# Performance work log

Measured on AMD Instinct MI355X. Metric: run time of the kernel, lower is better.

The kernel has to match this reference:

```python
import jax, jax.numpy as jnp
import numpy as np

B = 8192
W = 48            # target-net width
P = 4849          # flat param size of target MLP(1->48->48->48->1)
HW = 96           # hypernet width = 2*W
STEPS = 20
LR = 0.1
B1, B2, EPS = 0.9, 0.999, 1e-8


def setup_inputs() -> dict:
    key = jax.random.key(0)
    ks = jax.random.split(key, 6)
    x = jax.random.normal(ks[0], (B, 1), dtype=jnp.float32)
    c = jax.random.normal(ks[1], (B, 1), dtype=jnp.float32)
    # hypernet params (Linear(2,96) -> relu -> Linear(96,4849)), He-ish scaling
    hw1 = jax.random.normal(ks[2], (HW, 2), dtype=jnp.float32) / jnp.sqrt(2.0)
    hb1 = jax.random.normal(ks[3], (HW,), dtype=jnp.float32) * 0.1
    hw2 = jax.random.normal(ks[4], (P, HW), dtype=jnp.float32) / jnp.sqrt(float(HW))
    hb2 = jax.random.normal(ks[5], (P,), dtype=jnp.float32) * 0.1
    return {"x": x, "c": c, "hw1": hw1, "hb1": hb1, "hw2": hw2, "hb2": hb2}


def _target_apply(p, y):
    # unflatten per tree_flatten order: (w,b) per Linear layer of MLP(1,48,48,48,1)
    w0 = p[0:48].reshape(W, 1);      b0 = p[48:96]
    w1 = p[96:2400].reshape(W, W);   b1 = p[2400:2448]
    w2 = p[2448:4752].reshape(W, W); b2 = p[4752:4800]
    w3 = p[4800:4848].reshape(1, W); b3 = p[4848:4849]
    h = jax.nn.swish(w0 @ y + b0)
    h = jax.nn.swish(w1 @ h + b1)
    h = jax.nn.swish(w2 @ h + b2)
    return jnp.squeeze(w3 @ h + b3)


def _taylor_energy_y(energy_fn, y_target, y_anchor):
    # 2nd-order Taylor expansion via nested JVPs (order_y == 2)
    tangent = y_target - y_anchor

    def grad_energy(y):
        return jax.jvp(energy_fn, (y,), (tangent,))[1]

    e0, term1 = jax.jvp(energy_fn, (y_anchor,), (tangent,))
    _, term2 = jax.jvp(grad_energy, (y_anchor,), (tangent,))
    return e0 + term1 + 0.5 * term2


def _energy(y, p, y_anchor):
    return _taylor_energy_y(lambda yi: _target_apply(p, yi), y, y_anchor)


_grad_fn = jax.vmap(jax.grad(_energy), in_axes=(0, 0, 0))  # grad wrt y only


def reference(x, c, hw1, hb1, hw2, hb2):
    hyper_in = jnp.concatenate([x, c], axis=1)                 # (B, 2)
    h = jax.nn.relu(hyper_in @ hw1.T + hb1)                    # (B, 96)
    flat_params = h @ hw2.T + hb2                              # (B, P)

    y0 = jnp.zeros((x.shape[0], 1), dtype=x.dtype)             # y_mean = 0.0
    m0 = jnp.zeros_like(y0)
    v0 = jnp.zeros_like(y0)

    def step(carry, _):
        y, m, v, t = carry
        g = _grad_fn(y, flat_params, y)  # key=None -> anchor y0 = y_curr
        t = t + 1
        m = B1 * m + (1.0 - B1) * g
        v = B2 * v + (1.0 - B2) * g * g
        mh = m / (1.0 - jnp.power(B1, t))
        vh = v / (1.0 - jnp.power(B2, t))
        y = y - LR * mh / (jnp.sqrt(vh) + EPS)
        return (y, m, v, t), None

    (y_final, _, _, _), _ = jax.lax.scan(
        step, (y0, m0, v0, jnp.asarray(0, jnp.int32)), None, length=STEPS)
    return y_final
```

## Files before the change

kernel.cpp:

```cpp
#include <hip/hip_runtime.h>
#include <cstdint>
#include <cstddef>

#define NB    8192
#define NP    4849
#define NW    48
#define NCH   38
#define GY    16

typedef __attribute__((ext_vector_type(8))) _Float16 f16x8;
typedef __attribute__((ext_vector_type(4))) float f32x4;
typedef __attribute__((ext_vector_type(2))) float f32x2;

__device__ __forceinline__ const float* pptr(const float* Pp, int i, int rp) {
  return Pp + ((size_t)(rp >> 7) * NB + i) * 128 + (rp & 127);
}

__device__ __forceinline__ int invperm(int rp) {
  if (rp >= 96 && rp < 2400) {
    int t = rp - 96; int kb = t / 192; int rem = t - kb * 192;
    return 96 + (rem >> 2) * 48 + (kb * 4 + (rem & 3));
  }
  if (rp >= 2448 && rp < 4752) {
    int t = rp - 2448; int kb = t / 192; int rem = t - kb * 192;
    return 2448 + (rem >> 2) * 48 + (kb * 4 + (rem & 3));
  }
  return rp;
}

__global__ __launch_bounds__(256, 2) void hyper_gemm(
    const float* __restrict__ x, const float* __restrict__ c,
    const float* __restrict__ hw1, const float* __restrict__ hb1,
    const float* __restrict__ hw2, const float* __restrict__ hb2,
    float* __restrict__ Pp)
{
  const int t    = threadIdx.x;
  const int lane = t & 63;
  const int wv   = t >> 6;
  const int m16  = lane & 15;
  const int q    = lane >> 4;
  const int rp0  = blockIdx.x * 128;

  const float* wr[2];
  float bias[2];
  #pragma unroll
  for (int nt = 0; nt < 2; ++nt) {
    int rp = rp0 + wv * 32 + nt * 16 + m16;
    int r  = (rp < NP) ? invperm(rp) : 0;
    wr[nt]   = hw2 + (size_t)r * 96;
    bias[nt] = (rp < NP) ? hb2[r] : 0.f;
  }

  f16x8 bh[3][2], bl[3][2];
  #pragma unroll
  for (int ch = 0; ch < 3; ++ch) {
    const int k0 = ch * 32 + q * 8;
    #pragma unroll
    for (int nt = 0; nt < 2; ++nt) {
      float4 f0 = *(const float4*)(wr[nt] + k0);
      float4 f1 = *(const float4*)(wr[nt] + k0 + 4);
      float fv[8] = {f0.x,f0.y,f0.z,f0.w,f1.x,f1.y,f1.z,f1.w};
      #pragma unroll
      for (int e = 0; e < 8; ++e) {
        _Float16 hi = (_Float16)fv[e];
        float r = fv[e] - (float)hi;
        bh[ch][nt][e] = hi;
        bl[ch][nt][e] = (_Float16)r;
      }
    }
  }

  float* cbase = Pp + (size_t)blockIdx.x * NB * 128;

  for (int mtile = blockIdx.y; mtile < 128; mtile += GY) {
    const int i0 = mtile * 64;

    float xv[4], cv[4];
    #pragma unroll
    for (int mt = 0; mt < 4; ++mt) {
      int i = i0 + mt * 16 + m16;
      xv[mt] = x[i]; cv[mt] = c[i];
    }

    f32x4 acc[4][2];
    #pragma unroll
    for (int mt = 0; mt < 4; ++mt)
      #pragma unroll
      for (int nt = 0; nt < 2; ++nt)
        acc[mt][nt] = (f32x4){0.f, 0.f, 0.f, 0.f};

    #pragma unroll
    for (int ch = 0; ch < 3; ++ch) {
      const int k0 = ch * 32 + q * 8;

      float4 A0 = *(const float4*)(hw1 + 2 * k0);
      float4 A1 = *(const float4*)(hw1 + 2 * k0 + 4);
      float4 A2 = *(const float4*)(hw1 + 2 * k0 + 8);
      float4 A3 = *(const float4*)(hw1 + 2 * k0 + 12);
      float4 B0 = *(const float4*)(hb1 + k0);
      float4 B1 = *(const float4*)(hb1 + k0 + 4);
      float w0k[8] = {A0.x,A0.z,A1.x,A1.z,A2.x,A2.z,A3.x,A3.z};
      float w1k[8] = {A0.y,A0.w,A1.y,A1.w,A2.y,A2.w,A3.y,A3.w};
      float bk[8]  = {B0.x,B0.y,B0.z,B0.w,B1.x,B1.y,B1.z,B1.w};

      f16x8 ah[4], al[4];
      #pragma unroll
      for (int mt = 0; mt < 4; ++mt) {
        #pragma unroll
        for (int j = 0; j < 8; ++j) {
          float h = fmaf(xv[mt], w0k[j], fmaf(cv[mt], w1k[j], bk[j]));
          h = h > 0.f ? h : 0.f;
          _Float16 hi = (_Float16)h;
          float r = h - (float)hi;
          ah[mt][j] = hi;
          al[mt][j] = (_Float16)r;
        }
      }

      #pragma unroll
      for (int mt = 0; mt < 4; ++mt)
        #pragma unroll
        for (int nt = 0; nt < 2; ++nt) {
          acc[mt][nt] = __builtin_amdgcn_mfma_f32_16x16x32_f16(al[mt], bl[ch][nt], acc[mt][nt], 0, 0, 0);
          acc[mt][nt] = __builtin_amdgcn_mfma_f32_16x16x32_f16(ah[mt], bl[ch][nt], acc[mt][nt], 0, 0, 0);
          acc[mt][nt] = __builtin_amdgcn_mfma_f32_16x16x32_f16(al[mt], bh[ch][nt], acc[mt][nt], 0, 0, 0);
          acc[mt][nt] = __builtin_amdgcn_mfma_f32_16x16x32_f16(ah[mt], bh[ch][nt], acc[mt][nt], 0, 0, 0);
        }
    }

    #pragma unroll
    for (int nt = 0; nt < 2; ++nt) {
      int off = wv * 32 + nt * 16 + m16;
      if (rp0 + off < NP) {
        #pragma unroll
        for (int mt = 0; mt < 4; ++mt)
          #pragma unroll
          for (int r = 0; r < 4; ++r) {
            int i = i0 + mt * 16 + q * 4 + r;
            cbase[(size_t)i * 128 + off] = acc[mt][nt][r] + bias[nt];
          }
      }
    }
  }
}

__device__ __forceinline__ float rcp_nr(float d) {
  float r = __builtin_amdgcn_rcpf(d);
  return fmaf(-d, r, 2.f) * r;
}

#define DPP_ADD(x, ctrl, rmask)                                               \
  (x) += __int_as_float(__builtin_amdgcn_update_dpp(                          \
      0, __float_as_int(x), (ctrl), (rmask), 0xf, false))

__global__ __launch_bounds__(256, 2) void adam_inner(
    const float* __restrict__ Pp, float* __restrict__ out)
{
  __shared__ __align__(16) float hd[4][2][96];

  const int lane = threadIdx.x & 63;
  const int wv   = threadIdx.x >> 6;
  const int i    = blockIdx.x * 4 + wv;
  const bool act = lane < NW;

  float* buf0 = &hd[wv][0][0];
  float* buf1 = &hd[wv][1][0];

  float w0  = act ? *pptr(Pp, i, lane)        : 0.f;
  float b0  = act ? *pptr(Pp, i, 48 + lane)   : 0.f;
  float b1v = act ? *pptr(Pp, i, 2400 + lane) : 0.f;
  float b2v = act ? *pptr(Pp, i, 4752 + lane) : 0.f;
  float w3  = act ? *pptr(Pp, i, 4800 + lane) : 0.f;

  f32x2 w1p[24], w2p[24];
  #pragma unroll
  for (int kb = 0; kb < 12; ++kb) {
    float4 q1 = *(const float4*)pptr(Pp, i, 96 + kb * 192 + lane * 4);
    w1p[2 * kb]     = (f32x2){q1.x, q1.y};
    w1p[2 * kb + 1] = (f32x2){q1.z, q1.w};
    float4 q2 = *(const float4*)pptr(Pp, i, 2448 + kb * 192 + lane * 4);
    w2p[2 * kb]     = (f32x2){q2.x, q2.y};
    w2p[2 * kb + 1] = (f32x2){q2.z, q2.w};
  }

  float y = 0.f, m = 0.f, v = 0.f;
  float b1t = 1.f, b2t = 1.f;

  #pragma unroll 1
  for (int t = 0; t < 20; ++t) {
    float z  = fmaf(w0, y, b0);
    float e  = fminf(__expf(-z), 8.0e37f);
    float s  = rcp_nr(1.f + e);
    float h  = z * s;
    float dh = fmaf(z * s, 1.f - s, s) * w0;
    if (act) { buf0[lane] = h; buf0[48 + lane] = dh; }

    float4 ph[12], pd[12];
    #pragma unroll
    for (int kk = 0; kk < 12; ++kk) {
      ph[kk] = *(const float4*)(buf0 + 4 * kk);
      pd[kk] = *(const float4*)(buf0 + 48 + 4 * kk);
    }
    {
      f32x2 zz[4] = {(f32x2){b1v, 0.f}, (f32x2){0.f, 0.f},
                     (f32x2){0.f, 0.f}, (f32x2){0.f, 0.f}};
      f32x2 dd[4] = {(f32x2){0.f, 0.f}, (f32x2){0.f, 0.f},
                     (f32x2){0.f, 0.f}, (f32x2){0.f, 0.f}};
      #pragma unroll
      for (int kk = 0; kk < 12; ++kk) {
        int c0 = (2 * kk) & 3, c1 = (2 * kk + 1) & 3;
        zz[c0] = __builtin_elementwise_fma(w1p[2 * kk],     (f32x2){ph[kk].x, ph[kk].y}, zz[c0]);
        zz[c1] = __builtin_elementwise_fma(w1p[2 * kk + 1], (f32x2){ph[kk].z, ph[kk].w}, zz[c1]);
        dd[c0] = __builtin_elementwise_fma(w1p[2 * kk],     (f32x2){pd[kk].x, pd[kk].y}, dd[c0]);
        dd[c1] = __builtin_elementwise_fma(w1p[2 * kk + 1], (f32x2){pd[kk].z, pd[kk].w}, dd[c1]);
      }
      f32x2 zs = (zz[0] + zz[1]) + (zz[2] + zz[3]);
      f32x2 ds = (dd[0] + dd[1]) + (dd[2] + dd[3]);
      float z1  = zs.x + zs.y;
      float dz1 = ds.x + ds.y;

      e  = fminf(__expf(-z1), 8.0e37f);
      s  = rcp_nr(1.f + e);
      h  = z1 * s;
      dh = fmaf(z1 * s, 1.f - s, s) * dz1;
    }
    if (act) { buf1[lane] = h; buf1[48 + lane] = dh; }

    #pragma unroll
    for (int kk = 0; kk < 12; ++kk) {
      ph[kk] = *(const float4*)(buf1 + 4 * kk);
      pd[kk] = *(const float4*)(buf1 + 48 + 4 * kk);
    }
    {
      f32x2 zz[4] = {(f32x2){b2v, 0.f}, (f32x2){0.f, 0.f},
                     (f32x2){0.f, 0.f}, (f32x2){0.f, 0.f}};
      f32x2 dd[4] = {(f32x2){0.f, 0.f}, (f32x2){0.f, 0.f},
                     (f32x2){0.f, 0.f}, (f32x2){0.f, 0.f}};
      #pragma unroll
      for (int kk = 0; kk < 12; ++kk) {
        int c0 = (2 * kk) & 3, c1 = (2 * kk + 1) & 3;
        zz[c0] = __builtin_elementwise_fma(w2p[2 * kk],     (f32x2){ph[kk].x, ph[kk].y}, zz[c0]);
        zz[c1] = __builtin_elementwise_fma(w2p[2 * kk + 1], (f32x2){ph[kk].z, ph[kk].w}, zz[c1]);
        dd[c0] = __builtin_elementwise_fma(w2p[2 * kk],     (f32x2){pd[kk].x, pd[kk].y}, dd[c0]);
        dd[c1] = __builtin_elementwise_fma(w2p[2 * kk + 1], (f32x2){pd[kk].z, pd[kk].w}, dd[c1]);
      }
      f32x2 zs = (zz[0] + zz[1]) + (zz[2] + zz[3]);
      f32x2 ds = (dd[0] + dd[1]) + (dd[2] + dd[3]);
      float z2  = zs.x + zs.y;
      float dz2 = ds.x + ds.y;

      e  = fminf(__expf(-z2), 8.0e37f);
      s  = rcp_nr(1.f + e);
      dh = fmaf(z2 * s, 1.f - s, s) * dz2;
    }

    float r = act ? w3 * dh : 0.f;
    DPP_ADD(r, 0x111, 0xf);
    DPP_ADD(r, 0x112, 0xf);
    DPP_ADD(r, 0x114, 0xf);
    DPP_ADD(r, 0x118, 0xf);
    DPP_ADD(r, 0x142, 0xa);
    DPP_ADD(r, 0x143, 0xc);
    float g = __int_as_float(__builtin_amdgcn_readlane(__float_as_int(r), 63));

    m = fmaf(0.9f,   m, 0.1f   * g);
    v = fmaf(0.999f, v, 0.001f * g * g);
    b1t *= 0.9f; b2t *= 0.999f;
    float mh  = m * rcp_nr(1.f - b1t);
    float vh  = v * rcp_nr(1.f - b2t);
    float den = __builtin_amdgcn_sqrtf(vh) + 1e-8f;
    y -= 0.1f * mh * rcp_nr(den);
  }

  if (lane == 0) out[i] = y;
}

extern "C" void kernel_launch(void* const* d_in, const int* in_sizes, int n_in,
                              void* d_out, int out_size, void* d_ws, size_t ws_size,
                              hipStream_t stream) {
  const float* x   = (const float*)d_in[0];
  const float* c   = (const float*)d_in[1];
  const float* hw1 = (const float*)d_in[2];
  const float* hb1 = (const float*)d_in[3];
  const float* hw2 = (const float*)d_in[4];
  const float* hb2 = (const float*)d_in[5];
  float* Pp  = (float*)d_ws;
  float* out = (float*)d_out;

  dim3 gridB(NCH, GY);
  hyper_gemm<<<gridB, dim3(256), 0, stream>>>(x, c, hw1, hb1, hw2, hb2, Pp);
  adam_inner<<<dim3(2048), dim3(256), 0, stream>>>(Pp, out);
}
```

Before: 219.1 us.

## Process two samples per wavefront in the Adam inner loop to add ILP

Each wavefront now handles two batch samples at once, interleaving their layer computations so the two independent dependency chains can hide LDS and transcendental latency. The grid is halved to match. Newton-Raphson reciprocal refinement and the exp clamp are dropped in favour of raw rcp, and the bias-correction reciprocals are hoisted out of the per-sample loop. Register use roughly doubles for the weights (about 96 extra VGPRs), which with launch_bounds(256,2) risks spills or lower occupancy, and the raw rcp may slightly change numerics.

```diff
diff --git a/kernel.cpp b/kernel.cpp
--- a/kernel.cpp
+++ b/kernel.cpp
@@ -144,10 +144,6 @@
   }
 }
 
-__device__ __forceinline__ float rcp_nr(float d) {
-  float r = __builtin_amdgcn_rcpf(d);
-  return fmaf(-d, r, 2.f) * r;
-}
 
 #define DPP_ADD(x, ctrl, rmask)                                               \
   (x) += __int_as_float(__builtin_amdgcn_update_dpp(                          \
@@ -156,123 +152,123 @@
 __global__ __launch_bounds__(256, 2) void adam_inner(
     const float* __restrict__ Pp, float* __restrict__ out)
 {
-  __shared__ __align__(16) float hd[4][2][96];
+  __shared__ __align__(16) float hd[4][2][2][96];
 
   const int lane = threadIdx.x & 63;
   const int wv   = threadIdx.x >> 6;
-  const int i    = blockIdx.x * 4 + wv;
   const bool act = lane < NW;
 
-  float* buf0 = &hd[wv][0][0];
-  float* buf1 = &hd[wv][1][0];
-
-  float w0  = act ? *pptr(Pp, i, lane)        : 0.f;
-  float b0  = act ? *pptr(Pp, i, 48 + lane)   : 0.f;
-  float b1v = act ? *pptr(Pp, i, 2400 + lane) : 0.f;
-  float b2v = act ? *pptr(Pp, i, 4752 + lane) : 0.f;
-  float w3  = act ? *pptr(Pp, i, 4800 + lane) : 0.f;
-
-  f32x2 w1p[24], w2p[24];
+  float w0[2], b0[2], b1v[2], b2v[2], w3[2];
+  f32x2 w1p[2][24], w2p[2][24];
+
   #pragma unroll
-  for (int kb = 0; kb < 12; ++kb) {
-    float4 q1 = *(const float4*)pptr(Pp, i, 96 + kb * 192 + lane * 4);
-    w1p[2 * kb]     = (f32x2){q1.x, q1.y};
-    w1p[2 * kb + 1] = (f32x2){q1.z, q1.w};
-    float4 q2 = *(const float4*)pptr(Pp, i, 2448 + kb * 192 + lane * 4);
-    w2p[2 * kb]     = (f32x2){q2.x, q2.y};
-    w2p[2 * kb + 1] = (f32x2){q2.z, q2.w};
-  }
-
-  float y = 0.f, m = 0.f, v = 0.f;
+  for (int it = 0; it < 2; ++it) {
+    const int i = blockIdx.x * 8 + wv * 2 + it;
+    w0[it]  = act ? *pptr(Pp, i, lane)        : 0.f;
+    b0[it]  = act ? *pptr(Pp, i, 48 + lane)   : 0.f;
+    b1v[it] = act ? *pptr(Pp, i, 2400 + lane) : 0.f;
+    b2v[it] = act ? *pptr(Pp, i, 4752 + lane) : 0.f;
+    w3[it]  = act ? *pptr(Pp, i, 4800 + lane) : 0.f;
+    #pragma unroll
+    for (int kb = 0; kb < 12; ++kb) {
+      float4 q1 = *(const float4*)pptr(Pp, i, 96 + kb * 192 + lane * 4);
+      w1p[it][2 * kb]     = (f32x2){q1.x, q1.y};
+      w1p[it][2 * kb + 1] = (f32x2){q1.z, q1.w};
+      float4 q2 = *(const float4*)pptr(Pp, i, 2448 + kb * 192 + lane * 4);
+      w2p[it][2 * kb]     = (f32x2){q2.x, q2.y};
+      w2p[it][2 * kb + 1] = (f32x2){q2.z, q2.w};
+    }
+  }
+
+  float y[2] = {0.f, 0.f}, m[2] = {0.f, 0.f}, v[2] = {0.f, 0.f};
   float b1t = 1.f, b2t = 1.f;
 
   #pragma unroll 1
   for (int t = 0; t < 20; ++t) {
-    float z  = fmaf(w0, y, b0);
-    float e  = fminf(__expf(-z), 8.0e37f);
-    float s  = rcp_nr(1.f + e);
-    float h  = z * s;
-    float dh = fmaf(z * s, 1.f - s, s) * w0;
-    if (act) { buf0[lane] = h; buf0[48 + lane] = dh; }
-
-    float4 ph[12], pd[12];
+    #pragma unroll
+    for (int it = 0; it < 2; ++it) {
+      float z = fmaf(w0[it], y[it], b0[it]);
+      float s = __builtin_amdgcn_rcpf(1.f + __expf(-z));
+      float h = z * s;
+      float dh = fmaf(h, 1.f - s, s) * w0[it];
+      if (act) { hd[wv][it][0][lane] = h; hd[wv][it][0][48 + lane] = dh; }
+    }
+
+    f32x2 zz1[2] = {(f32x2){b1v[0], 0.f}, (f32x2){b1v[1], 0.f}};
+    f32x2 dd1[2] = {(f32x2){0.f, 0.f}, (f32x2){0.f, 0.f}};
     #pragma unroll
     for (int kk = 0; kk < 12; ++kk) {
-      ph[kk] = *(const float4*)(buf0 + 4 * kk);
-      pd[kk] = *(const float4*)(buf0 + 48 + 4 * kk);
-    }
-    {
-      f32x2 zz[4] = {(f32x2){b1v, 0.f}, (f32x2){0.f, 0.f},
-                     (f32x2){0.f, 0.f}, (f32x2){0.f, 0.f}};
-      f32x2 dd[4] = {(f32x2){0.f, 0.f}, (f32x2){0.f, 0.f},
-                     (f32x2){0.f, 0.f}, (f32x2){0.f, 0.f}};
-      #pragma unroll
-      for (int kk = 0; kk < 12; ++kk) {
-        int c0 = (2 * kk) & 3, c1 = (2 * kk + 1) & 3;
-        zz[c0] = __builtin_elementwise_fma(w1p[2 * kk],     (f32x2){ph[kk].x, ph[kk].y}, zz[c0]);
-        zz[c1] = __builtin_elementwise_fma(w1p[2 * kk + 1], (f32x2){ph[kk].z, ph[kk].w}, zz[c1]);
-        dd[c0] = __builtin_elementwise_fma(w1p[2 * kk],     (f32x2){pd[kk].x, pd[kk].y}, dd[c0]);
-        dd[c1] = __builtin_elementwise_fma(w1p[2 * kk + 1], (f32x2){pd[kk].z, pd[kk].w}, dd[c1]);
-      }
-      f32x2 zs = (zz[0] + zz[1]) + (zz[2] + zz[3]);
-      f32x2 ds = (dd[0] + dd[1]) + (dd[2] + dd[3]);
-      float z1  = zs.x + zs.y;
-      float dz1 = ds.x + ds.y;
-
-      e  = fminf(__expf(-z1), 8.0e37f);
-      s  = rcp_nr(1.f + e);
-      h  = z1 * s;
-      dh = fmaf(z1 * s, 1.f - s, s) * dz1;
-    }
-    if (act) { buf1[lane] = h; buf1[48 + lane] = dh; }
-
+      #pragma unroll
+      for (int it = 0; it < 2; ++it) {
+        float4 ph = *(const float4*)(&hd[wv][it][0][4 * kk]);
+        float4 pd = *(const float4*)(&hd[wv][it][0][48 + 4 * kk]);
+        zz1[it] = __builtin_elementwise_fma(w1p[it][2 * kk],     (f32x2){ph.x, ph.y}, zz1[it]);
+        zz1[it] = __builtin_elementwise_fma(w1p[it][2 * kk + 1], (f32x2){ph.z, ph.w}, zz1[it]);
+        dd1[it] = __builtin_elementwise_fma(w1p[it][2 * kk],     (f32x2){pd.x, pd.y}, dd1[it]);
+        dd1[it] = __builtin_elementwise_fma(w1p[it][2 * kk + 1], (f32x2){pd.z, pd.w}, dd1[it]);
+      }
+    }
+    #pragma unroll
+    for (int it = 0; it < 2; ++it) {
+      float z1  = zz1[it].x + zz1[it].y;
+      float dz1 = dd1[it].x + dd1[it].y;
+      float s = __builtin_amdgcn_rcpf(1.f + __expf(-z1));
+      float h = z1 * s;
+      float dh = fmaf(h, 1.f - s, s) * dz1;
+      if (act) { hd[wv][it][1][lane] = h; hd[wv][it][1][48 + lane] = dh; }
+    }
+
+    f32x2 zz2[2] = {(f32x2){b2v[0], 0.f}, (f32x2){b2v[1], 0.f}};
+    f32x2 dd2[2] = {(f32x2){0.f, 0.f}, (f32x2){0.f, 0.f}};
     #pragma unroll
     for (int kk = 0; kk < 12; ++kk) {
-      ph[kk] = *(const float4*)(buf1 + 4 * kk);
-      pd[kk] = *(const float4*)(buf1 + 48 + 4 * kk);
-    }
-    {
-      f32x2 zz[4] = {(f32x2){b2v, 0.f}, (f32x2){0.f, 0.f},
-                     (f32x2){0.f, 0.f}, (f32x2){0.f, 0.f}};
-      f32x2 dd[4] = {(f32x2){0.f, 0.f}, (f32x2){0.f, 0.f},
-                     (f32x2){0.f, 0.f}, (f32x2){0.f, 0.f}};
-      #pragma unroll
-      for (int kk = 0; kk < 12; ++kk) {
-        int c0 = (2 * kk) & 3, c1 = (2 * kk + 1) & 3;
-        zz[c0] = __builtin_elementwise_fma(w2p[2 * kk],     (f32x2){ph[kk].x, ph[kk].y}, zz[c0]);
-        zz[c1] = __builtin_elementwise_fma(w2p[2 * kk + 1], (f32x2){ph[kk].z, ph[kk].w}, zz[c1]);
-        dd[c0] = __builtin_elementwise_fma(w2p[2 * kk],     (f32x2){pd[kk].x, pd[kk].y}, dd[c0]);
-        dd[c1] = __builtin_elementwise_fma(w2p[2 * kk + 1], (f32x2){pd[kk].z, pd[kk].w}, dd[c1]);
-      }
-      f32x2 zs = (zz[0] + zz[1]) + (zz[2] + zz[3]);
-      f32x2 ds = (dd[0] + dd[1]) + (dd[2] + dd[3]);
-      float z2  = zs.x + zs.y;
-      float dz2 = ds.x + ds.y;
-
-      e  = fminf(__expf(-z2), 8.0e37f);
-      s  = rcp_nr(1.f + e);
-      dh = fmaf(z2 * s, 1.f - s, s) * dz2;
-    }
-
-    float r = act ? w3 * dh : 0.f;
-    DPP_ADD(r, 0x111, 0xf);
-    DPP_ADD(r, 0x112, 0xf);
-    DPP_ADD(r, 0x114, 0xf);
-    DPP_ADD(r, 0x118, 0xf);
-    DPP_ADD(r, 0x142, 0xa);
-    DPP_ADD(r, 0x143, 0xc);
-    float g = __int_as_float(__builtin_amdgcn_readlane(__float_as_int(r), 63));
-
-    m = fmaf(0.9f,   m, 0.1f   * g);
-    v = fmaf(0.999f, v, 0.001f * g * g);
+      #pragma unroll
+      for (int it = 0; it < 2; ++it) {
+        float4 ph = *(const float4*)(&hd[wv][it][1][4 * kk]);
+        float4 pd = *(const float4*)(&hd[wv][it][1][48 + 4 * kk]);
+        zz2[it] = __builtin_elementwise_fma(w2p[it][2 * kk],     (f32x2){ph.x, ph.y}, zz2[it]);
+        zz2[it] = __builtin_elementwise_fma(w2p[it][2 * kk + 1], (f32x2){ph.z, ph.w}, zz2[it]);
+        dd2[it] = __builtin_elementwise_fma(w2p[it][2 * kk],     (f32x2){pd.x, pd.y}, dd2[it]);
+        dd2[it] = __builtin_elementwise_fma(w2p[it][2 * kk + 1], (f32x2){pd.z, pd.w}, dd2[it]);
+      }
+    }
+
+    float g[2];
+    #pragma unroll
+    for (int it = 0; it < 2; ++it) {
+      float z2  = zz2[it].x + zz2[it].y;
+      float dz2 = dd2[it].x + dd2[it].y;
+      float s = __builtin_amdgcn_rcpf(1.f + __expf(-z2));
+      float dh = fmaf(z2 * s, 1.f - s, s) * dz2;
+
+      float r = act ? w3[it] * dh : 0.f;
+      DPP_ADD(r, 0x111, 0xf);
+      DPP_ADD(r, 0x112, 0xf);
+      DPP_ADD(r, 0x114, 0xf);
+      DPP_ADD(r, 0x118, 0xf);
+      DPP_ADD(r, 0x142, 0xa);
+      DPP_ADD(r, 0x143, 0xc);
+      g[it] = __int_as_float(__builtin_amdgcn_readlane(__float_as_int(r), 63));
+    }
+
     b1t *= 0.9f; b2t *= 0.999f;
-    float mh  = m * rcp_nr(1.f - b1t);
-    float vh  = v * rcp_nr(1.f - b2t);
-    float den = __builtin_amdgcn_sqrtf(vh) + 1e-8f;
-    y -= 0.1f * mh * rcp_nr(den);
-  }
-
-  if (lane == 0) out[i] = y;
+    float c1 = __builtin_amdgcn_rcpf(1.f - b1t);
+    float c2 = __builtin_amdgcn_rcpf(1.f - b2t);
+    #pragma unroll
+    for (int it = 0; it < 2; ++it) {
+      m[it] = fmaf(0.9f,   m[it], 0.1f   * g[it]);
+      v[it] = fmaf(0.999f, v[it], 0.001f * g[it] * g[it]);
+      float mh  = m[it] * c1;
+      float vh  = v[it] * c2;
+      float den = __builtin_amdgcn_sqrtf(vh) + 1e-8f;
+      y[it] -= 0.1f * mh * __builtin_amdgcn_rcpf(den);
+    }
+  }
+
+  if (lane == 0) {
+    out[blockIdx.x * 8 + wv * 2]     = y[0];
+    out[blockIdx.x * 8 + wv * 2 + 1] = y[1];
+  }
 }
 
 extern "C" void kernel_launch(void* const* d_in, const int* in_sizes, int n_in,
@@ -289,5 +285,5 @@
 
   dim3 gridB(NCH, GY);
   hyper_gemm<<<gridB, dim3(256), 0, stream>>>(x, c, hw1, hb1, hw2, hb2, Pp);
-  adam_inner<<<dim3(2048), dim3(256), 0, stream>>>(Pp, out);
-}
+  adam_inner<<<dim3(1024), dim3(256), 0, stream>>>(Pp, out);
+}
```

After: 629.2 us. +187.1%, slower.
